# Performance work log

Hardware: AMD Instinct MI355X
Metric: run time of the kernel (lower is better)

Reference implementation:

```python
import jax, jax.numpy as jnp
import numpy as np

BN_EPS = 1e-5

def _gin_mlp(h, wa, ba, wb, bb):
    # 2-layer MLP: Linear -> ReLU -> Linear
    return jax.nn.relu(h @ wa + ba) @ wb + bb

def _gin_conv(x, src, dst, n, wa, ba, wb, bb):
    # GIN aggregation: (1+eps)*x + sum_{j->i} x_j, eps=0 (PyG default)
    agg = jax.ops.segment_sum(x[src], dst, num_segments=n)
    return _gin_mlp(x + agg, wa, ba, wb, bb)

def _batchnorm(h, gamma, beta):
    # track_running_stats=False -> always batch stats, biased variance
    mean = jnp.mean(h, axis=0)
    var = jnp.var(h, axis=0)
    return (h - mean) * jax.lax.rsqrt(var + BN_EPS) * gamma + beta

def setup_inputs() -> dict:
    key = jax.random.key(0)
    ks = jax.random.split(key, 8)
    N, E, F, H, C = 100000, 1600000, 64, 64, 10
    s = 0.05
    return {
        "x": jax.random.normal(ks[0], (N, F), dtype=jnp.float32),
        "edge_index": jax.random.randint(ks[1], (2, E), 0, N, dtype=jnp.int64),
        "w1a": jax.random.normal(ks[2], (F, H), dtype=jnp.float32) * s,
        "b1a": jnp.zeros((H,), jnp.float32),
        "w1b": jax.random.normal(ks[3], (H, H), dtype=jnp.float32) * s,
        "b1b": jnp.zeros((H,), jnp.float32),
        "bn_gamma": jnp.ones((H,), jnp.float32),
        "bn_beta": jnp.zeros((H,), jnp.float32),
        "w2a": jax.random.normal(ks[4], (H, H), dtype=jnp.float32) * s,
        "b2a": jnp.zeros((H,), jnp.float32),
        "w2b": jax.random.normal(ks[5], (H, H), dtype=jnp.float32) * s,
        "b2b": jnp.zeros((H,), jnp.float32),
        "lin_w": jax.random.normal(ks[6], (H, C), dtype=jnp.float32) * s,
        "lin_b": jnp.zeros((C,), jnp.float32),
    }

def reference(x, edge_index, w1a, b1a, w1b, b1b, bn_gamma, bn_beta,
              w2a, b2a, w2b, b2b, lin_w, lin_b):
    n = x.shape[0]
    src, dst = edge_index[0], edge_index[1]
    h1 = _gin_conv(x, src, dst, n, w1a, b1a, w1b, b1b)   # [N, H]
    h1 = _batchnorm(h1, bn_gamma, bn_beta)               # relu1 never applied (faithful)
    h2 = _gin_conv(h1, src, dst, n, w2a, b2a, w2b, b2b)  # [N, H]
    return h2 @ lin_w + lin_b                            # [N, C]
```

## Files before the change

kernel.cpp:

```cpp
#include <hip/hip_runtime.h>
#include <hip/hip_fp16.h>

#define H 64
#define CBS 512
#define CB_BITS 9
#define TILE 8192
#define CAP 9216
#define NSTAT 64
#define RPK_BLKS 53

typedef _Float16 f16;
typedef __attribute__((ext_vector_type(8))) _Float16 v8h;
typedef __attribute__((ext_vector_type(4))) float v4f;

__global__ __launch_bounds__(256)
void init_kernel(int* __restrict__ gcursor, float* __restrict__ statsR, int CB) {
    int t = threadIdx.x;
    if (t < CB) gcursor[t * 16] = t * CAP;
    for (int i = t; i < NSTAT * 128; i += 256) statsR[i] = 0.f;
}

__global__ __launch_bounds__(256)
void front_kernel(const int* __restrict__ ei, int* __restrict__ gcursor,
                  int* __restrict__ pairs, int E, int N, int CB, int ntiles,
                  const float* __restrict__ x, f16* __restrict__ xh, int total4,
                  const float* __restrict__ W1a, const float* __restrict__ W1b,
                  const float* __restrict__ W2a, const float* __restrict__ W2b,
                  const float* __restrict__ B2b, const float* __restrict__ LW,
                  const float* __restrict__ LB,
                  f16* __restrict__ pk1a, f16* __restrict__ pk1b,
                  f16* __restrict__ pk2a, f16* __restrict__ pkf,
                  float* __restrict__ bf) {
    __shared__ int sd[256];
    __shared__ int excl[256];
    __shared__ int gbase[256];
    __shared__ int lcur[256];
    __shared__ int stage[TILE];
    __shared__ unsigned char bin8[TILE];
    int b = blockIdx.x;
    int t = threadIdx.x;

    if (b < ntiles) {
        int base = b * TILE;
        int cnt = min(TILE, E - base);
        sd[t] = 0;
        __syncthreads();
        for (int i = t; i < cnt; i += 256) {
            int s = ei[base + i];
            int d = ei[E + base + i];
            if ((unsigned)s < (unsigned)N && (unsigned)d < (unsigned)N)
                atomicAdd(&sd[d >> CB_BITS], 1);
        }
        __syncthreads();
        int v = sd[t];
        __syncthreads();
        for (int off = 1; off < 256; off <<= 1) {
            int add = (t >= off) ? sd[t - off] : 0;
            __syncthreads();
            sd[t] += add;
            __syncthreads();
        }
        int ex = sd[t] - v;
        excl[t] = ex;
        lcur[t] = ex;
        if (t < CB && v > 0) gbase[t] = atomicAdd(&gcursor[t * 16], v);
        int tot = sd[255];
        __syncthreads();
        for (int i = t; i < cnt; i += 256) {
            int s = ei[base + i];
            int d = ei[E + base + i];
            if ((unsigned)s < (unsigned)N && (unsigned)d < (unsigned)N) {
                int cb = d >> CB_BITS;
                int pos = atomicAdd(&lcur[cb], 1);
                stage[pos] = s | ((d & (CBS - 1)) << 17);
                bin8[pos] = (unsigned char)cb;
            }
        }
        __syncthreads();
        for (int i = t; i < tot; i += 256) {
            int b8 = bin8[i];
            pairs[gbase[b8] + (i - excl[b8])] = stage[i];
        }
        return;
    }
    b -= ntiles;
    if (b < RPK_BLKS) {
        int tt = b * 256 + t;
        if (tt < 12288) {
            int m = tt >> 12;
            int e = tt & 4095;
            int j = e & 7, lane = (e >> 3) & 63, ks = (e >> 9) & 1, nt = e >> 10;
            int row = ks * 32 + ((lane >> 4) & 3) * 8 + j;
            int col = nt * 16 + (lane & 15);
            const float* W = (m == 0) ? W1a : (m == 1) ? W1b : W2a;
            f16* P = (m == 0) ? pk1a : (m == 1) ? pk1b : pk2a;
            P[e] = (f16)W[row * 64 + col];
        } else if (tt < 13312) {
            int e = tt - 12288;
            int j = e & 7, lane = (e >> 3) & 63, ks = e >> 9;
            int row = ks * 32 + ((lane >> 4) & 3) * 8 + j;
            int col = lane & 15;
            float a = 0.f;
            if (col < 10)
                for (int m = 0; m < H; ++m) a = fmaf(W2b[row * 64 + m], LW[m * 10 + col], a);
            pkf[e] = (f16)a;
        } else if (tt < 13322) {
            int c = tt - 13312;
            float a = LB[c];
            for (int m = 0; m < H; ++m) a = fmaf(B2b[m], LW[m * 10 + c], a);
            bf[c] = a;
        }
        return;
    }
    b -= RPK_BLKS;
    int i = b * 256 + t;
    if (i >= total4) return;
    float4 v = ((const float4*)x)[i];
    f16 h0 = (f16)v.x, h1 = (f16)v.y, h2 = (f16)v.z, h3 = (f16)v.w;
    ushort4 pk;
    pk.x = *(unsigned short*)&h0; pk.y = *(unsigned short*)&h1;
    pk.z = *(unsigned short*)&h2; pk.w = *(unsigned short*)&h3;
    ((ushort4*)xh)[i] = pk;
}

__global__ __launch_bounds__(256)
void bucket_csr_kernel(const int* __restrict__ pairs, const int* __restrict__ gcursor,
                       int* __restrict__ ebuf, int* __restrict__ rowptr, int N, int CB) {
    __shared__ int hist[CBS];
    __shared__ int cur[CBS];
    __shared__ int sd[256];
    __shared__ int carry_s;
    int b = blockIdx.x;
    int t = threadIdx.x;
    int c_t = (t < CB) ? (gcursor[t * 16] - t * CAP) : 0;
    sd[t] = c_t; __syncthreads();
    for (int off = 1; off < 256; off <<= 1) {
        int add = (t >= off) ? sd[t - off] : 0;
        __syncthreads();
        sd[t] += add;
        __syncthreads();
    }
    int cnt = gcursor[b * 16] - b * CAP;
    int gb = sd[b] - cnt;
    if (b == 0 && t == 0) rowptr[N] = sd[255];
    __syncthreads();

    int pb = b * CAP;
    for (int i = t; i < CBS; i += 256) hist[i] = 0;
    if (t == 0) carry_s = 0;
    __syncthreads();
    for (int i = t; i < cnt; i += 256)
        atomicAdd(&hist[(pairs[pb + i] >> 17) & (CBS - 1)], 1);
    __syncthreads();
    for (int start = 0; start < CBS; start += 256) {
        int v = hist[start + t];
        sd[t] = v; __syncthreads();
        for (int off = 1; off < 256; off <<= 1) {
            int add = (t >= off) ? sd[t - off] : 0;
            __syncthreads();
            sd[t] += add;
            __syncthreads();
        }
        int ex = sd[t] - v + carry_s;
        cur[start + t] = ex;
        int node = b * CBS + start + t;
        if (node < N) rowptr[node] = gb + ex;
        __syncthreads();
        if (t == 0) carry_s += sd[255];
        __syncthreads();
    }
    for (int i = t; i < cnt; i += 256) {
        int p = pairs[pb + i];
        int pos = atomicAdd(&cur[(p >> 17) & (CBS - 1)], 1);
        ebuf[gb + pos] = p & 0x1FFFF;
    }
}

__global__ __launch_bounds__(256)
void g1mlp1_kernel(const f16* __restrict__ xh, const int* __restrict__ rowptr,
                   const int* __restrict__ ebuf, f16* __restrict__ h1p,
                   const f16* __restrict__ pk1a, const f16* __restrict__ pk1b,
                   const float* __restrict__ B1a, const float* __restrict__ B1b,
                   float* __restrict__ statsR, int N, int Em1) {
    __shared__ f16 agg[64][72];
    __shared__ f16 Su[4][16 * 72];
    __shared__ f16 Sh[4][16 * 72];
    __shared__ float red[2][4][64];
    int t = threadIdx.x, wv = t >> 6, lane = t & 63;
    int g = lane >> 3, fl = lane & 7;
    int node0 = blockIdx.x * 64;

#pragma unroll
    for (int r = 0; r < 2; ++r) {
        int nl = wv * 16 + r * 8 + g;
        int node = node0 + nl;
        bool vn = node < N;
        int p0 = 0, deg = 0;
        if (vn) {
            p0 = rowptr[node];
            deg = rowptr[node + 1] - p0;
        }
        int m = deg;
        m = max(m, __shfl_xor(m, 8));
        m = max(m, __shfl_xor(m, 16));
        m = max(m, __shfl_xor(m, 32));
        float a[8];
        {
            v8h s = {};
            if (vn) s = *(const v8h*)(xh + ((size_t)node << 6) + fl * 8);
#pragma unroll
            for (int j = 0; j < 8; ++j) a[j] = (float)s[j];
        }
        for (int k = 0; k < m; k += 4) {
            int idx[4];
#pragma unroll
            for (int q = 0; q < 4; ++q)
                idx[q] = ebuf[min(p0 + k + q, Em1)];
#pragma unroll
            for (int q = 0; q < 4; ++q) {
                if (k + q < deg) {
                    v8h v = *(const v8h*)(xh + ((size_t)idx[q] << 6) + fl * 8);
#pragma unroll
                    for (int j = 0; j < 8; ++j) a[j] += (float)v[j];
                }
            }
        }
        v8h o;
#pragma unroll
        for (int j = 0; j < 8; ++j) o[j] = (f16)a[j];
        *(v8h*)(&agg[nl][fl * 8]) = o;
    }
    __syncthreads();

    int quad = lane >> 4, r16 = lane & 15;
    int nodeA_l = wv * 16 + r16;
    v8h a0 = *(const v8h*)(&agg[nodeA_l][quad * 8]);
    v8h a1 = *(const v8h*)(&agg[nodeA_l][32 + quad * 8]);
#pragma unroll
    for (int nt = 0; nt < 4; ++nt) {
        v8h b0 = *(const v8h*)(pk1a + (((nt * 2 + 0) * 64 + lane) << 3));
        v8h b1 = *(const v8h*)(pk1a + (((nt * 2 + 1) * 64 + lane) << 3));
        v4f c = {0.f, 0.f, 0.f, 0.f};
        c = __builtin_amdgcn_mfma_f32_16x16x32_f16(a0, b0, c, 0, 0, 0);
        c = __builtin_amdgcn_mfma_f32_16x16x32_f16(a1, b1, c, 0, 0, 0);
        float bias = B1a[nt * 16 + r16];
#pragma unroll
        for (int reg = 0; reg < 4; ++reg)
            Su[wv][(quad * 4 + reg) * 72 + nt * 16 + r16] = (f16)fmaxf(c[reg] + bias, 0.f);
    }
    __syncthreads();
    v8h u0 = *(const v8h*)(&Su[wv][r16 * 72 + quad * 8]);
    v8h u1 = *(const v8h*)(&Su[wv][r16 * 72 + 32 + quad * 8]);
#pragma unroll
    for (int nt = 0; nt < 4; ++nt) {
        v8h b0 = *(const v8h*)(pk1b + (((nt * 2 + 0) * 64 + lane) << 3));
        v8h b1 = *(const v8h*)(pk1b + (((nt * 2 + 1) * 64 + lane) << 3));
        v4f c = {0.f, 0.f, 0.f, 0.f};
        c = __builtin_amdgcn_mfma_f32_16x16x32_f16(u0, b0, c, 0, 0, 0);
        c = __builtin_amdgcn_mfma_f32_16x16x32_f16(u1, b1, c, 0, 0, 0);
        float bias = B1b[nt * 16 + r16];
#pragma unroll
        for (int reg = 0; reg < 4; ++reg) {
            int row = quad * 4 + reg;
            bool valid = (node0 + wv * 16 + row) < N;
            Sh[wv][row * 72 + nt * 16 + r16] = valid ? (f16)(c[reg] + bias) : (f16)0;
        }
    }
    __syncthreads();
    int nbase = node0 + wv * 16;
    for (int i = lane; i < 1024; i += 64) {
        int row = i >> 6, col = i & 63;
        int node = nbase + row;
        if (node < N) h1p[(size_t)node * 64 + col] = Sh[wv][row * 72 + col];
    }
    float s = 0.f, s2 = 0.f;
#pragma unroll
    for (int row = 0; row < 16; ++row) {
        float v = (float)Sh[wv][row * 72 + lane];
        s += v;
        s2 = fmaf(v, v, s2);
    }
    red[0][wv][lane] = s;
    red[1][wv][lane] = s2;
    __syncthreads();
    if (wv == 0) {
        float ts  = (red[0][0][lane] + red[0][1][lane]) + (red[0][2][lane] + red[0][3][lane]);
        float ts2 = (red[1][0][lane] + red[1][1][lane]) + (red[1][2][lane] + red[1][3][lane]);
        float* st = statsR + (size_t)(blockIdx.x & (NSTAT - 1)) * 128;
        unsafeAtomicAdd(&st[lane], ts);
        unsafeAtomicAdd(&st[64 + lane], ts2);
    }
}

__global__ void bn_finalize_kernel(const float* __restrict__ statsR,
                                   const float* __restrict__ gamma,
                                   const float* __restrict__ beta,
                                   float* __restrict__ scale, float* __restrict__ shiftv, float n) {
    int f = threadIdx.x;
    if (f >= H) return;
    float s = 0.f, s2 = 0.f;
    for (int r = 0; r < NSTAT; ++r) {
        s  += statsR[r * 128 + f];
        s2 += statsR[r * 128 + 64 + f];
    }
    float mean = s / n;
    float var = s2 / n - mean * mean;
    var = fmaxf(var, 0.f);
    float sc = gamma[f] * rsqrtf(var + 1e-5f);
    scale[f] = sc;
    shiftv[f] = beta[f] - mean * sc;
}

__global__ __launch_bounds__(256)
void g2mlp2_kernel(const f16* __restrict__ h1p, const float* __restrict__ scale,
                   const float* __restrict__ shiftv, const int* __restrict__ rowptr,
                   const int* __restrict__ ebuf,
                   const f16* __restrict__ pk2a, const f16* __restrict__ pkf,
                   const float* __restrict__ B2a, const float* __restrict__ bf,
                   float* __restrict__ out, int N, int Em1) {
    __shared__ f16 agg[64][72];
    __shared__ f16 Su[4][16 * 72];
    int t = threadIdx.x, wv = t >> 6, lane = t & 63;
    int g = lane >> 3, fl = lane & 7;
    int node0 = blockIdx.x * 64;

    float sc[8], sh[8];
    {
        float4 s0 = *(const float4*)(scale + fl * 8);
        float4 s1 = *(const float4*)(scale + fl * 8 + 4);
        float4 h0 = *(const float4*)(shiftv + fl * 8);
        float4 h1 = *(const float4*)(shiftv + fl * 8 + 4);
        sc[0]=s0.x; sc[1]=s0.y; sc[2]=s0.z; sc[3]=s0.w;
        sc[4]=s1.x; sc[5]=s1.y; sc[6]=s1.z; sc[7]=s1.w;
        sh[0]=h0.x; sh[1]=h0.y; sh[2]=h0.z; sh[3]=h0.w;
        sh[4]=h1.x; sh[5]=h1.y; sh[6]=h1.z; sh[7]=h1.w;
    }

#pragma unroll
    for (int r = 0; r < 2; ++r) {
        int nl = wv * 16 + r * 8 + g;
        int node = node0 + nl;
        bool vn = node < N;
        int p0 = 0, deg = 0;
        if (vn) {
            p0 = rowptr[node];
            deg = rowptr[node + 1] - p0;
        }
        int m = deg;
        m = max(m, __shfl_xor(m, 8));
        m = max(m, __shfl_xor(m, 16));
        m = max(m, __shfl_xor(m, 32));
        float a[8];
        {
            v8h s = {};
            if (vn) s = *(const v8h*)(h1p + ((size_t)node << 6) + fl * 8);
#pragma unroll
            for (int j = 0; j < 8; ++j) a[j] = (float)s[j];
        }
        for (int k = 0; k < m; k += 4) {
            int idx[4];
#pragma unroll
            for (int q = 0; q < 4; ++q)
                idx[q] = ebuf[min(p0 + k + q, Em1)];
#pragma unroll
            for (int q = 0; q < 4; ++q) {
                if (k + q < deg) {
                    v8h v = *(const v8h*)(h1p + ((size_t)idx[q] << 6) + fl * 8);
#pragma unroll
                    for (int j = 0; j < 8; ++j) a[j] += (float)v[j];
                }
            }
        }
        float degp1 = (float)(deg + 1);
        v8h o;
#pragma unroll
        for (int j = 0; j < 8; ++j) o[j] = (f16)(a[j] * sc[j] + degp1 * sh[j]);
        *(v8h*)(&agg[nl][fl * 8]) = o;
    }
    __syncthreads();

    int quad = lane >> 4, r16 = lane & 15;
    int nodeA_l = wv * 16 + r16;
    v8h a0 = *(const v8h*)(&agg[nodeA_l][quad * 8]);
    v8h a1 = *(const v8h*)(&agg[nodeA_l][32 + quad * 8]);
#pragma unroll
    for (int nt = 0; nt < 4; ++nt) {
        v8h b0 = *(const v8h*)(pk2a + (((nt * 2 + 0) * 64 + lane) << 3));
        v8h b1 = *(const v8h*)(pk2a + (((nt * 2 + 1) * 64 + lane) << 3));
        v4f c = {0.f, 0.f, 0.f, 0.f};
        c = __builtin_amdgcn_mfma_f32_16x16x32_f16(a0, b0, c, 0, 0, 0);
        c = __builtin_amdgcn_mfma_f32_16x16x32_f16(a1, b1, c, 0, 0, 0);
        float bias = B2a[nt * 16 + r16];
#pragma unroll
        for (int reg = 0; reg < 4; ++reg)
            Su[wv][(quad * 4 + reg) * 72 + nt * 16 + r16] = (f16)fmaxf(c[reg] + bias, 0.f);
    }
    __syncthreads();
    v8h u0 = *(const v8h*)(&Su[wv][r16 * 72 + quad * 8]);
    v8h u1 = *(const v8h*)(&Su[wv][r16 * 72 + 32 + quad * 8]);
    v8h b0 = *(const v8h*)(pkf + ((0 * 64 + lane) << 3));
    v8h b1 = *(const v8h*)(pkf + ((1 * 64 + lane) << 3));
    v4f c = {0.f, 0.f, 0.f, 0.f};
    c = __builtin_amdgcn_mfma_f32_16x16x32_f16(u0, b0, c, 0, 0, 0);
    c = __builtin_amdgcn_mfma_f32_16x16x32_f16(u1, b1, c, 0, 0, 0);
    if (r16 < 10) {
        float bias = bf[r16];
#pragma unroll
        for (int reg = 0; reg < 4; ++reg) {
            int node = node0 + wv * 16 + quad * 4 + reg;
            if (node < N) out[(size_t)node * 10 + r16] = c[reg] + bias;
        }
    }
}

extern "C" void kernel_launch(void* const* d_in, const int* in_sizes, int n_in,
                              void* d_out, int out_size, void* d_ws, size_t ws_size,
                              hipStream_t stream) {
    const float* x    = (const float*)d_in[0];
    const int*   ei   = (const int*)d_in[1];
    const float* w1a  = (const float*)d_in[2];
    const float* b1a  = (const float*)d_in[3];
    const float* w1b  = (const float*)d_in[4];
    const float* b1b  = (const float*)d_in[5];
    const float* bng  = (const float*)d_in[6];
    const float* bnb  = (const float*)d_in[7];
    const float* w2a  = (const float*)d_in[8];
    const float* b2a  = (const float*)d_in[9];
    const float* w2b  = (const float*)d_in[10];
    const float* b2b  = (const float*)d_in[11];
    const float* linw = (const float*)d_in[12];
    const float* linb = (const float*)d_in[13];

    int N = in_sizes[0] / H;
    int E = in_sizes[1] / 2;
    int CB = (N + CBS - 1) / CBS;

    size_t NH = (size_t)N * H;
    char*  wsb    = (char*)d_ws;
    f16*   xh     = (f16*)wsb;
    f16*   h1p    = (f16*)(wsb + NH * 2);
    float* stats  = (float*)(wsb + NH * 6);
    float* scale  = stats + 128;
    float* shiftv = stats + 192;
    float* bf     = stats + 256;
    f16*   pk1a   = (f16*)(bf + 16);
    f16*   pk1b   = pk1a + 4096;
    f16*   pk2a   = pk1b + 4096;
    f16*   pkf    = pk2a + 4096;
    int*   gcursor= (int*)(pkf + 1024);
    int*   rowptr = gcursor + 256 * 16;
    int*   ebuf   = rowptr + (N + 1);
    int*   pairs  = ebuf + E;
    float* statsR = (float*)(pairs + (size_t)CB * CAP);

    int ntiles = (E + TILE - 1) / TILE;
    int total4 = (int)(NH / 4);
    int cvtblocks = (total4 + 255) / 256;
    int mblocks = (N + 63) / 64;

    init_kernel<<<1, 256, 0, stream>>>(gcursor, statsR, CB);
    front_kernel<<<ntiles + RPK_BLKS + cvtblocks, 256, 0, stream>>>(
        ei, gcursor, pairs, E, N, CB, ntiles,
        x, xh, total4,
        w1a, w1b, w2a, w2b, b2b, linw, linb,
        pk1a, pk1b, pk2a, pkf, bf);
    bucket_csr_kernel<<<CB, 256, 0, stream>>>(pairs, gcursor, ebuf, rowptr, N, CB);
    g1mlp1_kernel<<<mblocks, 256, 0, stream>>>(
        xh, rowptr, ebuf, h1p, pk1a, pk1b, b1a, b1b, statsR, N, E - 1);
    bn_finalize_kernel<<<1, 64, 0, stream>>>(statsR, bng, bnb, scale, shiftv, (float)N);
    g2mlp2_kernel<<<mblocks, 256, 0, stream>>>(
        h1p, scale, shiftv, rowptr, ebuf, pk2a, pkf, b2a, bf, (float*)d_out, N, E - 1);
}
```

Measured before the change: 246.1 us.

## Split fused gather+MLP kernels into separate gather and MLP kernels

Each fused gather+MLP kernel is split into a standalone gather kernel, which writes aggregated fp16 features to a global buffer, and an MLP kernel that reads them back. The gather loop now unrolls by 8 with a fast path that skips bounds checks. It also drops the per-wave max-degree loop, so each 8-lane group stops at its own node's degree. This aims to raise occupancy and memory-level parallelism in the gather, since the MFMA stage and its shared memory no longer sit in the same kernel. The cost is two extra launches and an extra global write and read of N×64 fp16 per layer. mlp1 writes h1 in place into the same buffer it reads; each wave reads its own rows before writing them, so this looks safe.

```diff
diff --git a/kernel.cpp b/kernel.cpp
--- a/kernel.cpp
+++ b/kernel.cpp
@@ -177,65 +177,139 @@
 }
 
 __global__ __launch_bounds__(256)
-void g1mlp1_kernel(const f16* __restrict__ xh, const int* __restrict__ rowptr,
-                   const int* __restrict__ ebuf, f16* __restrict__ h1p,
-                   const f16* __restrict__ pk1a, const f16* __restrict__ pk1b,
-                   const float* __restrict__ B1a, const float* __restrict__ B1b,
-                   float* __restrict__ statsR, int N, int Em1) {
-    __shared__ f16 agg[64][72];
+void gather1_kernel(const f16* __restrict__ xh, const int* __restrict__ rowptr,
+                    const int* __restrict__ ebuf, f16* __restrict__ bufA,
+                    int N, int Em1) {
+    int wid = (int)(((long long)blockIdx.x * blockDim.x + threadIdx.x) >> 6);
+    int lane = threadIdx.x & 63;
+    int g = lane >> 3, fl = lane & 7;
+    int node = wid * 8 + g;
+    bool vn = node < N;
+    int p0 = 0, deg = 0;
+    if (vn) {
+        p0 = rowptr[node];
+        deg = rowptr[node + 1] - p0;
+    }
+    float a[8];
+    {
+        v8h s = {};
+        if (vn) s = *(const v8h*)(xh + ((size_t)node << 6) + fl * 8);
+#pragma unroll
+        for (int j = 0; j < 8; ++j) a[j] = (float)s[j];
+    }
+    int k = 0;
+    for (; k + 8 <= deg; k += 8) {
+        int idx[8];
+#pragma unroll
+        for (int q = 0; q < 8; ++q) idx[q] = ebuf[p0 + k + q];
+#pragma unroll
+        for (int q = 0; q < 8; ++q) {
+            v8h v = *(const v8h*)(xh + ((size_t)idx[q] << 6) + fl * 8);
+#pragma unroll
+            for (int j = 0; j < 8; ++j) a[j] += (float)v[j];
+        }
+    }
+    if (k < deg) {
+        int idx[8];
+#pragma unroll
+        for (int q = 0; q < 8; ++q) idx[q] = ebuf[min(p0 + k + q, Em1)];
+#pragma unroll
+        for (int q = 0; q < 8; ++q) {
+            if (k + q < deg) {
+                v8h v = *(const v8h*)(xh + ((size_t)idx[q] << 6) + fl * 8);
+#pragma unroll
+                for (int j = 0; j < 8; ++j) a[j] += (float)v[j];
+            }
+        }
+    }
+    if (vn) {
+        v8h o;
+#pragma unroll
+        for (int j = 0; j < 8; ++j) o[j] = (f16)a[j];
+        *(v8h*)(bufA + ((size_t)node << 6) + fl * 8) = o;
+    }
+}
+
+__global__ __launch_bounds__(256)
+void gather2_kernel(const f16* __restrict__ h1p, const float* __restrict__ scale,
+                    const float* __restrict__ shiftv, const int* __restrict__ rowptr,
+                    const int* __restrict__ ebuf, f16* __restrict__ bufC,
+                    int N, int Em1) {
+    int wid = (int)(((long long)blockIdx.x * blockDim.x + threadIdx.x) >> 6);
+    int lane = threadIdx.x & 63;
+    int g = lane >> 3, fl = lane & 7;
+    int node = wid * 8 + g;
+    bool vn = node < N;
+    int p0 = 0, deg = 0;
+    if (vn) {
+        p0 = rowptr[node];
+        deg = rowptr[node + 1] - p0;
+    }
+    float a[8];
+    {
+        v8h s = {};
+        if (vn) s = *(const v8h*)(h1p + ((size_t)node << 6) + fl * 8);
+#pragma unroll
+        for (int j = 0; j < 8; ++j) a[j] = (float)s[j];
+    }
+    int k = 0;
+    for (; k + 8 <= deg; k += 8) {
+        int idx[8];
+#pragma unroll
+        for (int q = 0; q < 8; ++q) idx[q] = ebuf[p0 + k + q];
+#pragma unroll
+        for (int q = 0; q < 8; ++q) {
+            v8h v = *(const v8h*)(h1p + ((size_t)idx[q] << 6) + fl * 8);
+#pragma unroll
+            for (int j = 0; j < 8; ++j) a[j] += (float)v[j];
+        }
+    }
+    if (k < deg) {
+        int idx[8];
+#pragma unroll
+        for (int q = 0; q < 8; ++q) idx[q] = ebuf[min(p0 + k + q, Em1)];
+#pragma unroll
+        for (int q = 0; q < 8; ++q) {
+            if (k + q < deg) {
+                v8h v = *(const v8h*)(h1p + ((size_t)idx[q] << 6) + fl * 8);
+#pragma unroll
+                for (int j = 0; j < 8; ++j) a[j] += (float)v[j];
+            }
+        }
+    }
+    if (vn) {
+        float4 s0 = *(const float4*)(scale + fl * 8);
+        float4 s1 = *(const float4*)(scale + fl * 8 + 4);
+        float4 h0 = *(const float4*)(shiftv + fl * 8);
+        float4 h1 = *(const float4*)(shiftv + fl * 8 + 4);
+        float degp1 = (float)(deg + 1);
+        float sc[8] = {s0.x, s0.y, s0.z, s0.w, s1.x, s1.y, s1.z, s1.w};
+        float sh[8] = {h0.x, h0.y, h0.z, h0.w, h1.x, h1.y, h1.z, h1.w};
+        v8h o;
+#pragma unroll
+        for (int j = 0; j < 8; ++j) o[j] = (f16)(a[j] * sc[j] + degp1 * sh[j]);
+        *(v8h*)(bufC + ((size_t)node << 6) + fl * 8) = o;
+    }
+}
+
+__global__ __launch_bounds__(256)
+void mlp1_kernel(const f16* __restrict__ bufA, f16* __restrict__ h1p,
+                 const f16* __restrict__ pk1a, const f16* __restrict__ pk1b,
+                 const float* __restrict__ B1a, const float* __restrict__ B1b,
+                 float* __restrict__ statsR, int N) {
     __shared__ f16 Su[4][16 * 72];
     __shared__ f16 Sh[4][16 * 72];
     __shared__ float red[2][4][64];
     int t = threadIdx.x, wv = t >> 6, lane = t & 63;
-    int g = lane >> 3, fl = lane & 7;
-    int node0 = blockIdx.x * 64;
-
-#pragma unroll
-    for (int r = 0; r < 2; ++r) {
-        int nl = wv * 16 + r * 8 + g;
-        int node = node0 + nl;
-        bool vn = node < N;
-        int p0 = 0, deg = 0;
-        if (vn) {
-            p0 = rowptr[node];
-            deg = rowptr[node + 1] - p0;
-        }
-        int m = deg;
-        m = max(m, __shfl_xor(m, 8));
-        m = max(m, __shfl_xor(m, 16));
-        m = max(m, __shfl_xor(m, 32));
-        float a[8];
-        {
-            v8h s = {};
-            if (vn) s = *(const v8h*)(xh + ((size_t)node << 6) + fl * 8);
-#pragma unroll
-            for (int j = 0; j < 8; ++j) a[j] = (float)s[j];
-        }
-        for (int k = 0; k < m; k += 4) {
-            int idx[4];
-#pragma unroll
-            for (int q = 0; q < 4; ++q)
-                idx[q] = ebuf[min(p0 + k + q, Em1)];
-#pragma unroll
-            for (int q = 0; q < 4; ++q) {
-                if (k + q < deg) {
-                    v8h v = *(const v8h*)(xh + ((size_t)idx[q] << 6) + fl * 8);
-#pragma unroll
-                    for (int j = 0; j < 8; ++j) a[j] += (float)v[j];
-                }
-            }
-        }
-        v8h o;
-#pragma unroll
-        for (int j = 0; j < 8; ++j) o[j] = (f16)a[j];
-        *(v8h*)(&agg[nl][fl * 8]) = o;
-    }
-    __syncthreads();
-
     int quad = lane >> 4, r16 = lane & 15;
-    int nodeA_l = wv * 16 + r16;
-    v8h a0 = *(const v8h*)(&agg[nodeA_l][quad * 8]);
-    v8h a1 = *(const v8h*)(&agg[nodeA_l][32 + quad * 8]);
+    int node0 = blockIdx.x * 64 + wv * 16;
+    int nodeA = node0 + r16;
+
+    v8h a0 = {}, a1 = {};
+    if (nodeA < N) {
+        a0 = *(const v8h*)(bufA + (size_t)nodeA * 64 + quad * 8);
+        a1 = *(const v8h*)(bufA + (size_t)nodeA * 64 + 32 + quad * 8);
+    }
 #pragma unroll
     for (int nt = 0; nt < 4; ++nt) {
         v8h b0 = *(const v8h*)(pk1a + (((nt * 2 + 0) * 64 + lane) << 3));
@@ -262,15 +336,14 @@
 #pragma unroll
         for (int reg = 0; reg < 4; ++reg) {
             int row = quad * 4 + reg;
-            bool valid = (node0 + wv * 16 + row) < N;
+            bool valid = (node0 + row) < N;
             Sh[wv][row * 72 + nt * 16 + r16] = valid ? (f16)(c[reg] + bias) : (f16)0;
         }
     }
     __syncthreads();
-    int nbase = node0 + wv * 16;
     for (int i = lane; i < 1024; i += 64) {
         int row = i >> 6, col = i & 63;
-        int node = nbase + row;
+        int node = node0 + row;
         if (node < N) h1p[(size_t)node * 64 + col] = Sh[wv][row * 72 + col];
     }
     float s = 0.f, s2 = 0.f;
@@ -312,77 +385,21 @@
 }
 
 __global__ __launch_bounds__(256)
-void g2mlp2_kernel(const f16* __restrict__ h1p, const float* __restrict__ scale,
-                   const float* __restrict__ shiftv, const int* __restrict__ rowptr,
-                   const int* __restrict__ ebuf,
-                   const f16* __restrict__ pk2a, const f16* __restrict__ pkf,
-                   const float* __restrict__ B2a, const float* __restrict__ bf,
-                   float* __restrict__ out, int N, int Em1) {
-    __shared__ f16 agg[64][72];
+void mlp2_kernel(const f16* __restrict__ bufC,
+                 const f16* __restrict__ pk2a, const f16* __restrict__ pkf,
+                 const float* __restrict__ B2a, const float* __restrict__ bf,
+                 float* __restrict__ out, int N) {
     __shared__ f16 Su[4][16 * 72];
     int t = threadIdx.x, wv = t >> 6, lane = t & 63;
-    int g = lane >> 3, fl = lane & 7;
-    int node0 = blockIdx.x * 64;
-
-    float sc[8], sh[8];
-    {
-        float4 s0 = *(const float4*)(scale + fl * 8);
-        float4 s1 = *(const float4*)(scale + fl * 8 + 4);
-        float4 h0 = *(const float4*)(shiftv + fl * 8);
-        float4 h1 = *(const float4*)(shiftv + fl * 8 + 4);
-        sc[0]=s0.x; sc[1]=s0.y; sc[2]=s0.z; sc[3]=s0.w;
-        sc[4]=s1.x; sc[5]=s1.y; sc[6]=s1.z; sc[7]=s1.w;
-        sh[0]=h0.x; sh[1]=h0.y; sh[2]=h0.z; sh[3]=h0.w;
-        sh[4]=h1.x; sh[5]=h1.y; sh[6]=h1.z; sh[7]=h1.w;
-    }
-
-#pragma unroll
-    for (int r = 0; r < 2; ++r) {
-        int nl = wv * 16 + r * 8 + g;
-        int node = node0 + nl;
-        bool vn = node < N;
-        int p0 = 0, deg = 0;
-        if (vn) {
-            p0 = rowptr[node];
-            deg = rowptr[node + 1] - p0;
-        }
-        int m = deg;
-        m = max(m, __shfl_xor(m, 8));
-        m = max(m, __shfl_xor(m, 16));
-        m = max(m, __shfl_xor(m, 32));
-        float a[8];
-        {
-            v8h s = {};
-            if (vn) s = *(const v8h*)(h1p + ((size_t)node << 6) + fl * 8);
-#pragma unroll
-            for (int j = 0; j < 8; ++j) a[j] = (float)s[j];
-        }
-        for (int k = 0; k < m; k += 4) {
-            int idx[4];
-#pragma unroll
-            for (int q = 0; q < 4; ++q)
-                idx[q] = ebuf[min(p0 + k + q, Em1)];
-#pragma unroll
-            for (int q = 0; q < 4; ++q) {
-                if (k + q < deg) {
-                    v8h v = *(const v8h*)(h1p + ((size_t)idx[q] << 6) + fl * 8);
-#pragma unroll
-                    for (int j = 0; j < 8; ++j) a[j] += (float)v[j];
-                }
-            }
-        }
-        float degp1 = (float)(deg + 1);
-        v8h o;
-#pragma unroll
-        for (int j = 0; j < 8; ++j) o[j] = (f16)(a[j] * sc[j] + degp1 * sh[j]);
-        *(v8h*)(&agg[nl][fl * 8]) = o;
-    }
-    __syncthreads();
-
     int quad = lane >> 4, r16 = lane & 15;
-    int nodeA_l = wv * 16 + r16;
-    v8h a0 = *(const v8h*)(&agg[nodeA_l][quad * 8]);
-    v8h a1 = *(const v8h*)(&agg[nodeA_l][32 + quad * 8]);
+    int node0 = blockIdx.x * 64 + wv * 16;
+    int nodeA = node0 + r16;
+
+    v8h a0 = {}, a1 = {};
+    if (nodeA < N) {
+        a0 = *(const v8h*)(bufC + (size_t)nodeA * 64 + quad * 8);
+        a1 = *(const v8h*)(bufC + (size_t)nodeA * 64 + 32 + quad * 8);
+    }
 #pragma unroll
     for (int nt = 0; nt < 4; ++nt) {
         v8h b0 = *(const v8h*)(pk2a + (((nt * 2 + 0) * 64 + lane) << 3));
@@ -407,7 +424,7 @@
         float bias = bf[r16];
 #pragma unroll
         for (int reg = 0; reg < 4; ++reg) {
-            int node = node0 + wv * 16 + quad * 4 + reg;
+            int node = node0 + quad * 4 + reg;
             if (node < N) out[(size_t)node * 10 + r16] = c[reg] + bias;
         }
     }
@@ -438,7 +455,8 @@
     size_t NH = (size_t)N * H;
     char*  wsb    = (char*)d_ws;
     f16*   xh     = (f16*)wsb;
-    f16*   h1p    = (f16*)(wsb + NH * 2);
+    f16*   bufA   = (f16*)(wsb + NH * 2);
+    f16*   bufC   = (f16*)(wsb + NH * 4);
     float* stats  = (float*)(wsb + NH * 6);
     float* scale  = stats + 128;
     float* shiftv = stats + 192;
@@ -457,6 +475,8 @@
     int total4 = (int)(NH / 4);
     int cvtblocks = (total4 + 255) / 256;
     int mblocks = (N + 63) / 64;
+    int nwaves = (N + 7) / 8;
+    int gblocks = (int)(((long long)nwaves * 64 + 255) / 256);
 
     init_kernel<<<1, 256, 0, stream>>>(gcursor, statsR, CB);
     front_kernel<<<ntiles + RPK_BLKS + cvtblocks, 256, 0, stream>>>(
@@ -465,9 +485,11 @@
         w1a, w1b, w2a, w2b, b2b, linw, linb,
         pk1a, pk1b, pk2a, pkf, bf);
     bucket_csr_kernel<<<CB, 256, 0, stream>>>(pairs, gcursor, ebuf, rowptr, N, CB);
-    g1mlp1_kernel<<<mblocks, 256, 0, stream>>>(
-        xh, rowptr, ebuf, h1p, pk1a, pk1b, b1a, b1b, statsR, N, E - 1);
+
+    gather1_kernel<<<gblocks, 256, 0, stream>>>(xh, rowptr, ebuf, bufA, N, E - 1);
+    mlp1_kernel<<<mblocks, 256, 0, stream>>>(bufA, bufA, pk1a, pk1b, b1a, b1b, statsR, N);
     bn_finalize_kernel<<<1, 64, 0, stream>>>(statsR, bng, bnb, scale, shiftv, (float)N);
-    g2mlp2_kernel<<<mblocks, 256, 0, stream>>>(
-        h1p, scale, shiftv, rowptr, ebuf, pk2a, pkf, b2a, bf, (float*)d_out, N, E - 1);
-}
+
+    gather2_kernel<<<gblocks, 256, 0, stream>>>(bufA, scale, shiftv, rowptr, ebuf, bufC, N, E - 1);
+    mlp2_kernel<<<mblocks, 256, 0, stream>>>(bufC, pk2a, pkf, b2a, bf, (float*)d_out, N);
+}
```

New measurement: 232.4 us. -5.5%, faster.
